# Kernel tuning notes

Hardware: AMD Instinct MI355X
Metric: run time of the kernel (lower is better)

Reference implementation:

```python
import jax, jax.numpy as jnp
import numpy as np

B, T = 16, 2048
OBS_DIM, ACT_DIM, HIDDEN = 64, 16, 512


def setup_inputs() -> dict:
    key = jax.random.key(0)
    ks = jax.random.split(key, 6)
    n = lambda k, shape, scale: (jax.random.normal(k, shape, dtype=jnp.float32) * scale)
    return {
        "obs": n(ks[0], (B, T, OBS_DIM), 1.0),
        "act": n(ks[1], (B, T, ACT_DIM), 1.0),
        "W_e": n(ks[2], (HIDDEN, OBS_DIM + ACT_DIM), 0.05),   # embed Linear weight
        "b_e": jnp.zeros((HIDDEN,), jnp.float32),             # embed Linear bias
        "a_raw": n(ks[3], (HIDDEN,), 0.5),                    # diagonal decay (pre-tanh)
        "W_B": n(ks[4], (HIDDEN, HIDDEN), 0.02),              # B Linear weight (no bias)
        "W_out": n(ks[5], (OBS_DIM, HIDDEN), 0.04),           # out Linear weight
        "b_out": jnp.zeros((OBS_DIM,), jnp.float32),          # out Linear bias
    }


def reference(obs, act, W_e, b_e, a_raw, W_B, W_out, b_out):
    # x: [B, T, obs+act]
    x = jnp.concatenate([obs, act], axis=-1)
    # embed: Linear + ReLU, batched over all timesteps -> u: [B, T, H]
    u = jax.nn.relu(jnp.einsum('btd,hd->bth', x, W_e) + b_e)
    # B projection batched over all t (the per-step matmul in the torch loop)
    v = jnp.einsum('bth,gh->btg', u, W_B)  # [B, T, H]
    a = jnp.tanh(a_raw)  # [H]
    # Diagonal linear recurrence s_t = a * s_{t-1} + v_t, s_0 starting from zeros,
    # realized as a parallel (log-depth) associative scan over (decay, input) pairs.
    A = jnp.broadcast_to(a, v.shape)
    def combine(c1, c2):
        a1, b1 = c1
        a2, b2 = c2
        return (a1 * a2, a2 * b1 + b2)
    _, s = jax.lax.associative_scan(combine, (A, v), axis=1)  # s: [B, T, H]
    # out projection per step -> preds: [B, T, obs_dim]
    return jnp.einsum('bth,oh->bto', s, W_out) + b_out
```

## Files before the change

kernel.cpp:

```cpp
#include <hip/hip_runtime.h>
#include <hip/hip_bf16.h>

#define B_    16
#define T_    2048
#define H_    512
#define BT_   32768
#define DIN   80
#define DPAD  128
#define L_    64
#define C_    32
#define O_    64
#define NCHUNK (BT_ / L_)

typedef __attribute__((ext_vector_type(8))) short short8;
typedef __attribute__((ext_vector_type(4))) float f32x4;
typedef __attribute__((ext_vector_type(4))) float float4v;

__device__ __forceinline__ float bf2f(unsigned short u) {
  union { unsigned int i; float f; } x; x.i = ((unsigned int)u) << 16; return x.f;
}
__device__ __forceinline__ unsigned short f2bf(float f) {
  union { float f; unsigned int i; } x; x.f = f;
  unsigned int r = x.i + 0x7fffu + ((x.i >> 16) & 1u);
  return (unsigned short)(r >> 16);
}

template<int NT, int RELU, int BIAS, int CE>
__global__ __launch_bounds__(512) void gemm256(
    const unsigned short* __restrict__ A, const unsigned short* __restrict__ Bt,
    const float* __restrict__ bias, unsigned short* __restrict__ Cb,
    int ldk,
    const float* __restrict__ powa,
    float* __restrict__ e)
{
  __shared__ __align__(16) unsigned char lds[131072];

  const int tid  = threadIdx.x;
  const int lane = tid & 63;
  const int wid  = tid >> 6;
  const int wr   = wid >> 2;
  const int wc   = wid & 3;
  const int cl   = lane & 15;
  const int kgrp = lane >> 4;
  const int rg   = kgrp * 4;

  const int X  = (int)blockIdx.x & 7;
  const int j  = (int)blockIdx.x >> 3;
  const int mt = X * 16 + (j >> 1);
  const int nt = j & 1;
  const int row0 = mt * 256, col0 = nt * 256;

  auto stageA = [&](int q, int buf) {
    const int k0 = q * 64;
    #pragma unroll
    for (int r = 0; r < 4; ++r) {
      const int o   = r * 8192 + tid * 16;
      const int row = o >> 7;
      const int c16 = (o >> 4) & 7;
      const int kk  = (c16 ^ (row & 7)) << 3;
      __builtin_amdgcn_global_load_lds(
          (const __attribute__((address_space(1))) void*)
              (A + (size_t)(row0 + row) * ldk + k0 + kk),
          (__attribute__((address_space(3))) void*)(lds + buf * 65536 + o),
          16, 0, 0);
    }
  };
  auto stageB = [&](int q, int buf) {
    const int k0 = q * 64;
    #pragma unroll
    for (int r = 0; r < 4; ++r) {
      const int o   = r * 8192 + tid * 16;
      const int col = o >> 7;
      const int c16 = (o >> 4) & 7;
      const int kk  = (c16 ^ (col & 7)) << 3;
      __builtin_amdgcn_global_load_lds(
          (const __attribute__((address_space(1))) void*)
              (Bt + (size_t)(col0 + col) * ldk + k0 + kk),
          (__attribute__((address_space(3))) void*)(lds + buf * 65536 + 32768 + o),
          16, 0, 0);
    }
  };

  f32x4 acc[8][4];
  #pragma unroll
  for (int m = 0; m < 8; ++m)
    #pragma unroll
    for (int n = 0; n < 4; ++n) acc[m][n] = f32x4{0.f, 0.f, 0.f, 0.f};

  stageA(0, 0); stageB(0, 0); stageB(1, 1);
  asm volatile("s_waitcnt vmcnt(4)" ::: "memory");
  __builtin_amdgcn_sched_barrier(0);
  __builtin_amdgcn_s_barrier();

  for (int q = 0; q < NT; ++q) {
    const int cur = q & 1;
    const unsigned char* bufp = lds + cur * 65536;

    if (q + 1 < NT) stageA(q + 1, cur ^ 1);

    short8 bfr[4][2];
    #pragma unroll
    for (int n = 0; n < 4; ++n) {
      const int col = wc * 64 + n * 16 + cl;
      #pragma unroll
      for (int ks = 0; ks < 2; ++ks)
        bfr[n][ks] = *(const short8*)(bufp + 32768 + col * 128 +
                                      ((((ks << 2) + kgrp) ^ (col & 7)) << 4));
    }
    asm volatile("s_waitcnt lgkmcnt(0)" ::: "memory");
    __builtin_amdgcn_sched_barrier(0);
    __builtin_amdgcn_s_barrier();

    if (q + 2 < NT) stageB(q + 2, cur);

    #pragma unroll
    for (int g = 0; g < 4; ++g) {
      short8 af[2][2];
      #pragma unroll
      for (int mm = 0; mm < 2; ++mm) {
        const int row = wr * 128 + (g * 2 + mm) * 16 + cl;
        #pragma unroll
        for (int ks = 0; ks < 2; ++ks)
          af[mm][ks] = *(const short8*)(bufp + row * 128 +
                                        ((((ks << 2) + kgrp) ^ (row & 7)) << 4));
      }
      #pragma unroll
      for (int ks = 0; ks < 2; ++ks)
        #pragma unroll
        for (int mm = 0; mm < 2; ++mm)
          #pragma unroll
          for (int n = 0; n < 4; ++n)
            acc[g * 2 + mm][n] = __builtin_amdgcn_mfma_f32_16x16x32_bf16(
                af[mm][ks], bfr[n][ks], acc[g * 2 + mm][n], 0, 0, 0);
    }

    if (q + 2 < NT) {
      asm volatile("s_waitcnt vmcnt(4)" ::: "memory");
    } else if (q + 1 < NT) {
      asm volatile("s_waitcnt vmcnt(0)" ::: "memory");
    }
    __builtin_amdgcn_sched_barrier(0);
    __builtin_amdgcn_s_barrier();
  }

  #pragma unroll
  for (int m = 0; m < 8; ++m) {
    #pragma unroll
    for (int n = 0; n < 4; ++n) {
      const int gc = col0 + wc * 64 + n * 16 + cl;
      #pragma unroll
      for (int e2 = 0; e2 < 4; ++e2) {
        const int gr = row0 + wr * 128 + m * 16 + rg + e2;
        float v = acc[m][n][e2];
        if (BIAS) v += bias[gc];
        if (RELU) v = fmaxf(v, 0.f);
        Cb[(size_t)gr * H_ + gc] = f2bf(v);
      }
    }
  }

  if (CE) {
    #pragma unroll
    for (int c = 0; c < 2; ++c) {
      const int chunk = ((row0 + wr * 128) >> 6) + c;
      #pragma unroll
      for (int n = 0; n < 4; ++n) {
        const int h = col0 + wc * 64 + n * 16 + cl;
        const float a16 = powa[15 * H_ + h];
        float ep = 0.f;
        #pragma unroll
        for (int e2 = 0; e2 < 4; ++e2) {
          const int k = 15 - rg - e2;
          const float wk = (k == 0) ? 1.f : powa[(size_t)(k - 1) * H_ + h];
          float hsum = acc[c * 4 + 0][n][e2];
          hsum = fmaf(hsum, a16, acc[c * 4 + 1][n][e2]);
          hsum = fmaf(hsum, a16, acc[c * 4 + 2][n][e2]);
          hsum = fmaf(hsum, a16, acc[c * 4 + 3][n][e2]);
          ep = fmaf(wk, hsum, ep);
        }
        ep += __shfl_xor(ep, 16);
        ep += __shfl_xor(ep, 32);
        if (kgrp == 0)
          e[(size_t)chunk * H_ + h] = ep;
      }
    }
  }
}

#define PX_N  (BT_ * 16)
#define WE_N  (H_ * DPAD)
#define WB_N  (H_ * H_)
#define WO_N  (O_ * H_)
#define PW_N  (WE_N + WB_N + WO_N + H_)
#define PREP_THREADS (PX_N + PW_N)

__global__ __launch_bounds__(256) void prep(
    const float* __restrict__ obs, const float* __restrict__ act,
    const float* __restrict__ W_e, const float* __restrict__ W_B,
    const float* __restrict__ W_out, const float* __restrict__ a_raw,
    unsigned short* __restrict__ xb,
    unsigned short* __restrict__ Web, unsigned short* __restrict__ WBb,
    unsigned short* __restrict__ Woutb, float* __restrict__ aarr,
    float* __restrict__ powa)
{
  const int gid = blockIdx.x * 256 + threadIdx.x;
  if (gid < PX_N) {
    const int g = gid & 15, n = gid >> 4;
    float f[8];
    if (g < 8) {
      const float4v f0 = ((const float4v*)obs)[(size_t)n * 16 + g * 2];
      const float4v f1 = ((const float4v*)obs)[(size_t)n * 16 + g * 2 + 1];
      f[0]=f0[0]; f[1]=f0[1]; f[2]=f0[2]; f[3]=f0[3];
      f[4]=f1[0]; f[5]=f1[1]; f[6]=f1[2]; f[7]=f1[3];
    } else if (g < 10) {
      const float4v f0 = ((const float4v*)act)[(size_t)n * 4 + (g - 8) * 2];
      const float4v f1 = ((const float4v*)act)[(size_t)n * 4 + (g - 8) * 2 + 1];
      f[0]=f0[0]; f[1]=f0[1]; f[2]=f0[2]; f[3]=f0[3];
      f[4]=f1[0]; f[5]=f1[1]; f[6]=f1[2]; f[7]=f1[3];
    } else {
      #pragma unroll
      for (int i = 0; i < 8; ++i) f[i] = 0.f;
    }
    short8 o;
    #pragma unroll
    for (int i = 0; i < 8; ++i) o[i] = (short)f2bf(f[i]);
    *(short8*)(xb + (size_t)gid * 8) = o;
    return;
  }
  const int idx = gid - PX_N;
  if (idx < WE_N) {
    const int h = idx >> 7, d = idx & 127;
    Web[idx] = f2bf(d < DIN ? W_e[h * DIN + d] : 0.f);
  } else if (idx < WE_N + WB_N) {
    const int j = idx - WE_N;
    WBb[j] = f2bf(W_B[j]);
  } else if (idx < WE_N + WB_N + WO_N) {
    const int j = idx - (WE_N + WB_N);
    Woutb[j] = f2bf(W_out[j]);
  } else if (idx < PW_N) {
    const int h = idx - (WE_N + WB_N + WO_N);
    const float a = tanhf(a_raw[h]);
    aarr[h] = a;
    float p = a;
    #pragma unroll
    for (int i = 0; i < 16; ++i) { powa[i * H_ + h] = p; p *= a; }
  }
}

__global__ __launch_bounds__(256) void scan_out(
    const unsigned int* __restrict__ v,
    const float* __restrict__ e,
    const float* __restrict__ aarr,
    const unsigned short* __restrict__ Wo,
    const float* __restrict__ b_out,
    float* __restrict__ y)
{
  __shared__ __align__(16) unsigned char sbytes[64 * 1024];
  const int blk = blockIdx.x;
  const int b = blk >> 5, c = blk & 31;
  const int tid = threadIdx.x;
  const int lane = tid & 63, w = tid >> 6;
  const int row_base = blk * L_;

  {
    const int h0 = tid * 2;
    const float a0 = aarr[h0], a1 = aarr[h0 + 1];
    float aL0 = a0 * a0, aL1 = a1 * a1;
    aL0 *= aL0; aL1 *= aL1;
    aL0 *= aL0; aL1 *= aL1;
    aL0 *= aL0; aL1 *= aL1;
    aL0 *= aL0; aL1 *= aL1;
    aL0 *= aL0; aL1 *= aL1;
    float s0 = 0.f, s1 = 0.f;
    for (int j = 0; j < c; ++j) {
      const size_t o = ((size_t)(b * C_ + j)) * H_ + h0;
      s0 = fmaf(aL0, s0, e[o]);
      s1 = fmaf(aL1, s1, e[o + 1]);
    }
    const unsigned int* vp = v + (size_t)row_base * (H_ / 2) + tid;
    #pragma unroll 8
    for (int t = 0; t < L_; ++t) {
      const unsigned int pv = vp[(size_t)t * (H_ / 2)];
      s0 = fmaf(a0, s0, bf2f((unsigned short)(pv & 0xffff)));
      s1 = fmaf(a1, s1, bf2f((unsigned short)(pv >> 16)));
      const int byte = t * 1024 + ((tid * 4) ^ ((t & 7) << 4));
      *(unsigned int*)(sbytes + byte) =
          (unsigned int)f2bf(s0) | ((unsigned int)f2bf(s1) << 16);
    }
  }
  __syncthreads();

  f32x4 acc[4];
  #pragma unroll
  for (int n = 0; n < 4; ++n) acc[n] = f32x4{0.f, 0.f, 0.f, 0.f};
  const int r = w * 16 + (lane & 15);
  const int kof = (lane >> 4) * 8;
  #pragma unroll 4
  for (int k0 = 0; k0 < H_; k0 += 32) {
    const int byte = r * 1024 + (((k0 + kof) * 2) ^ ((r & 7) << 4));
    const short8 af = *(const short8*)(sbytes + byte);
    #pragma unroll
    for (int n = 0; n < 4; ++n) {
      const short8 bf = *(const short8*)(Wo + (size_t)(n * 16 + (lane & 15)) * H_ + k0 + kof);
      acc[n] = __builtin_amdgcn_mfma_f32_16x16x32_bf16(af, bf, acc[n], 0, 0, 0);
    }
  }
  const int cl = lane & 15, rg = (lane >> 4) * 4;
  #pragma unroll
  for (int n = 0; n < 4; ++n) {
    #pragma unroll
    for (int e2 = 0; e2 < 4; ++e2) {
      const int gr = row_base + w * 16 + rg + e2;
      const int gc = n * 16 + cl;
      y[(size_t)gr * O_ + gc] = acc[n][e2] + b_out[gc];
    }
  }
}

extern "C" void kernel_launch(void* const* d_in, const int* in_sizes, int n_in,
                              void* d_out, int out_size, void* d_ws, size_t ws_size,
                              hipStream_t stream)
{
  const float* obs   = (const float*)d_in[0];
  const float* act   = (const float*)d_in[1];
  const float* W_e   = (const float*)d_in[2];
  const float* b_e   = (const float*)d_in[3];
  const float* a_raw = (const float*)d_in[4];
  const float* W_B   = (const float*)d_in[5];
  const float* W_out = (const float*)d_in[6];
  const float* b_out = (const float*)d_in[7];
  float* y = (float*)d_out;

  char* w = (char*)d_ws;
  auto carve = [&](size_t bytes) {
    char* p = w; w += (bytes + 255) & ~(size_t)255; return p;
  };
  unsigned short* xb    = (unsigned short*)carve((size_t)BT_ * DPAD * 2);
  unsigned short* Web   = (unsigned short*)carve((size_t)H_ * DPAD * 2);
  unsigned short* WBb   = (unsigned short*)carve((size_t)H_ * H_ * 2);
  unsigned short* Woutb = (unsigned short*)carve((size_t)O_ * H_ * 2);
  float*          aarr  = (float*)carve((size_t)H_ * 4);
  float*          powa  = (float*)carve((size_t)16 * H_ * 4);
  unsigned short* u     = (unsigned short*)carve((size_t)BT_ * H_ * 2);
  unsigned short* v     = (unsigned short*)carve((size_t)BT_ * H_ * 2);
  float*          e     = (float*)carve((size_t)NCHUNK * H_ * 4);

  prep<<<PREP_THREADS / 256, 256, 0, stream>>>(obs, act, W_e, W_B, W_out,
                                               a_raw, xb, Web, WBb, Woutb,
                                               aarr, powa);
  gemm256<2, 1, 1, 0><<<256, 512, 0, stream>>>(
      xb, Web, b_e, u, DPAD, nullptr, nullptr);
  gemm256<8, 0, 0, 1><<<256, 512, 0, stream>>>(
      u, WBb, nullptr, v, H_, powa, e);
  scan_out<<<NCHUNK, 256, 0, stream>>>((const unsigned int*)v, e, aarr,
                                       Woutb, b_out, y);
}
```

Baseline: 75.52 us.

## Fuse input conversion into embed GEMM, add carry-scan kernel, interleave B loads

The separate obs/act-to-bf16 prep pass and its xb buffer are removed. The embed GEMM now reads fp32 obs/act directly, converts them into swizzled LDS, and loads both K-tiles of W_e up front. The B-projection GEMM splits its B staging into per-round loads interleaved with the MFMA groups and raises wave priority around the compute. A new carry_scan kernel computes the per-chunk prefix states once, replacing the O(C) serial loop in every scan_out block, at the cost of an extra launch and buffer.

```diff
diff --git a/kernel.cpp b/kernel.cpp
--- a/kernel.cpp
+++ b/kernel.cpp
@@ -25,14 +25,13 @@
   return (unsigned short)(r >> 16);
 }
 
-template<int NT, int RELU, int BIAS, int CE>
-__global__ __launch_bounds__(512) void gemm256(
+__global__ __launch_bounds__(512) void gemm_bproj(
     const unsigned short* __restrict__ A, const unsigned short* __restrict__ Bt,
-    const float* __restrict__ bias, unsigned short* __restrict__ Cb,
-    int ldk,
+    unsigned short* __restrict__ Cb,
     const float* __restrict__ powa,
     float* __restrict__ e)
 {
+  constexpr int NT = 8;
   __shared__ __align__(16) unsigned char lds[131072];
 
   const int tid  = threadIdx.x;
@@ -60,13 +59,204 @@
       const int kk  = (c16 ^ (row & 7)) << 3;
       __builtin_amdgcn_global_load_lds(
           (const __attribute__((address_space(1))) void*)
-              (A + (size_t)(row0 + row) * ldk + k0 + kk),
+              (A + (size_t)(row0 + row) * H_ + k0 + kk),
           (__attribute__((address_space(3))) void*)(lds + buf * 65536 + o),
           16, 0, 0);
     }
   };
-  auto stageB = [&](int q, int buf) {
+  auto stageB_round = [&](int q, int buf, int r) {
     const int k0 = q * 64;
+    const int o   = r * 8192 + tid * 16;
+    const int col = o >> 7;
+    const int c16 = (o >> 4) & 7;
+    const int kk  = (c16 ^ (col & 7)) << 3;
+    __builtin_amdgcn_global_load_lds(
+        (const __attribute__((address_space(1))) void*)
+            (Bt + (size_t)(col0 + col) * H_ + k0 + kk),
+        (__attribute__((address_space(3))) void*)(lds + buf * 65536 + 32768 + o),
+        16, 0, 0);
+  };
+
+  f32x4 acc[8][4];
+  #pragma unroll
+  for (int m = 0; m < 8; ++m)
+    #pragma unroll
+    for (int n = 0; n < 4; ++n) acc[m][n] = f32x4{0.f, 0.f, 0.f, 0.f};
+
+  stageA(0, 0);
+  #pragma unroll
+  for (int r = 0; r < 4; ++r) stageB_round(0, 0, r);
+  #pragma unroll
+  for (int r = 0; r < 4; ++r) stageB_round(1, 1, r);
+  asm volatile("s_waitcnt vmcnt(4)" ::: "memory");
+  __builtin_amdgcn_sched_barrier(0);
+  __builtin_amdgcn_s_barrier();
+
+  for (int q = 0; q < NT; ++q) {
+    const int cur = q & 1;
+    const unsigned char* bufp = lds + cur * 65536;
+
+    if (q + 1 < NT) stageA(q + 1, cur ^ 1);
+
+    short8 bfr[4][2];
+    #pragma unroll
+    for (int n = 0; n < 4; ++n) {
+      const int col = wc * 64 + n * 16 + cl;
+      #pragma unroll
+      for (int ks = 0; ks < 2; ++ks)
+        bfr[n][ks] = *(const short8*)(bufp + 32768 + col * 128 +
+                                      ((((ks << 2) + kgrp) ^ (col & 7)) << 4));
+    }
+    asm volatile("s_waitcnt lgkmcnt(0)" ::: "memory");
+    __builtin_amdgcn_sched_barrier(0);
+    __builtin_amdgcn_s_barrier();
+
+    __builtin_amdgcn_s_setprio(1);
+    #pragma unroll
+    for (int g = 0; g < 4; ++g) {
+      if (q + 2 < NT) stageB_round(q + 2, cur, g);
+      short8 af[2][2];
+      #pragma unroll
+      for (int mm = 0; mm < 2; ++mm) {
+        const int row = wr * 128 + (g * 2 + mm) * 16 + cl;
+        #pragma unroll
+        for (int ks = 0; ks < 2; ++ks)
+          af[mm][ks] = *(const short8*)(bufp + row * 128 +
+                                        ((((ks << 2) + kgrp) ^ (row & 7)) << 4));
+      }
+      #pragma unroll
+      for (int ks = 0; ks < 2; ++ks)
+        #pragma unroll
+        for (int mm = 0; mm < 2; ++mm)
+          #pragma unroll
+          for (int n = 0; n < 4; ++n)
+            acc[g * 2 + mm][n] = __builtin_amdgcn_mfma_f32_16x16x32_bf16(
+                af[mm][ks], bfr[n][ks], acc[g * 2 + mm][n], 0, 0, 0);
+    }
+    __builtin_amdgcn_s_setprio(0);
+
+    if (q + 2 < NT) {
+      asm volatile("s_waitcnt vmcnt(4)" ::: "memory");
+    } else if (q + 1 < NT) {
+      asm volatile("s_waitcnt vmcnt(0)" ::: "memory");
+    }
+    __builtin_amdgcn_sched_barrier(0);
+    __builtin_amdgcn_s_barrier();
+  }
+
+  #pragma unroll
+  for (int m = 0; m < 8; ++m) {
+    #pragma unroll
+    for (int n = 0; n < 4; ++n) {
+      const int gc = col0 + wc * 64 + n * 16 + cl;
+      #pragma unroll
+      for (int e2 = 0; e2 < 4; ++e2) {
+        const int gr = row0 + wr * 128 + m * 16 + rg + e2;
+        Cb[(size_t)gr * H_ + gc] = f2bf(acc[m][n][e2]);
+      }
+    }
+  }
+
+  #pragma unroll
+  for (int c = 0; c < 2; ++c) {
+    const int chunk = ((row0 + wr * 128) >> 6) + c;
+    #pragma unroll
+    for (int n = 0; n < 4; ++n) {
+      const int h = col0 + wc * 64 + n * 16 + cl;
+      const float a16 = powa[15 * H_ + h];
+      float ep = 0.f;
+      #pragma unroll
+      for (int e2 = 0; e2 < 4; ++e2) {
+        const int k = 15 - rg - e2;
+        const float wk = (k == 0) ? 1.f : powa[(size_t)(k - 1) * H_ + h];
+        float hsum = acc[c * 4 + 0][n][e2];
+        hsum = fmaf(hsum, a16, acc[c * 4 + 1][n][e2]);
+        hsum = fmaf(hsum, a16, acc[c * 4 + 2][n][e2]);
+        hsum = fmaf(hsum, a16, acc[c * 4 + 3][n][e2]);
+        ep = fmaf(wk, hsum, ep);
+      }
+      ep += __shfl_xor(ep, 16);
+      ep += __shfl_xor(ep, 32);
+      if (kgrp == 0)
+        e[(size_t)chunk * H_ + h] = ep;
+    }
+  }
+}
+
+__global__ __launch_bounds__(512) void embed_gemm(
+    const float* __restrict__ obs, const float* __restrict__ act,
+    const unsigned short* __restrict__ Web,
+    const float* __restrict__ b_e,
+    unsigned short* __restrict__ u)
+{
+  __shared__ __align__(16) unsigned char lds[131072];
+
+  const int tid  = threadIdx.x;
+  const int lane = tid & 63;
+  const int wid  = tid >> 6;
+  const int wr   = wid >> 2;
+  const int wc   = wid & 3;
+  const int cl   = lane & 15;
+  const int kgrp = lane >> 4;
+  const int rg   = kgrp * 4;
+
+  const int X  = (int)blockIdx.x & 7;
+  const int j  = (int)blockIdx.x >> 3;
+  const int mt = X * 16 + (j >> 1);
+  const int nt = j & 1;
+  const int row0 = mt * 256, col0 = nt * 256;
+
+  {
+    const int row  = tid >> 1;
+    const int half = tid & 1;
+    {
+      const float4v* src = (const float4v*)(obs + (size_t)(row0 + row) * 64 + half * 32);
+      float f[32];
+      #pragma unroll
+      for (int i = 0; i < 8; ++i) {
+        const float4v t4 = src[i];
+        f[i*4+0]=t4[0]; f[i*4+1]=t4[1]; f[i*4+2]=t4[2]; f[i*4+3]=t4[3];
+      }
+      #pragma unroll
+      for (int cc = 0; cc < 4; ++cc) {
+        short8 o8;
+        #pragma unroll
+        for (int jj = 0; jj < 8; ++jj) o8[jj] = (short)f2bf(f[cc*8+jj]);
+        const int c16 = half * 4 + cc;
+        *(short8*)(lds + row * 128 + ((c16 ^ (row & 7)) << 4)) = o8;
+      }
+    }
+    {
+      short8 z8;
+      #pragma unroll
+      for (int jj = 0; jj < 8; ++jj) z8[jj] = 0;
+      if (half == 0) {
+        const float4v* asrc = (const float4v*)(act + (size_t)(row0 + row) * 16);
+        float g[16];
+        #pragma unroll
+        for (int i = 0; i < 4; ++i) {
+          const float4v t4 = asrc[i];
+          g[i*4+0]=t4[0]; g[i*4+1]=t4[1]; g[i*4+2]=t4[2]; g[i*4+3]=t4[3];
+        }
+        #pragma unroll
+        for (int cc = 0; cc < 2; ++cc) {
+          short8 o8;
+          #pragma unroll
+          for (int jj = 0; jj < 8; ++jj) o8[jj] = (short)f2bf(g[cc*8+jj]);
+          *(short8*)(lds + 65536 + row * 128 + ((cc ^ (row & 7)) << 4)) = o8;
+        }
+        #pragma unroll
+        for (int cc = 2; cc < 4; ++cc)
+          *(short8*)(lds + 65536 + row * 128 + ((cc ^ (row & 7)) << 4)) = z8;
+      } else {
+        #pragma unroll
+        for (int cc = 4; cc < 8; ++cc)
+          *(short8*)(lds + 65536 + row * 128 + ((cc ^ (row & 7)) << 4)) = z8;
+      }
+    }
+  }
+  #pragma unroll
+  for (int q = 0; q < 2; ++q) {
     #pragma unroll
     for (int r = 0; r < 4; ++r) {
       const int o   = r * 8192 + tid * 16;
@@ -75,11 +265,12 @@
       const int kk  = (c16 ^ (col & 7)) << 3;
       __builtin_amdgcn_global_load_lds(
           (const __attribute__((address_space(1))) void*)
-              (Bt + (size_t)(col0 + col) * ldk + k0 + kk),
-          (__attribute__((address_space(3))) void*)(lds + buf * 65536 + 32768 + o),
+              (Web + (size_t)(col0 + col) * DPAD + q * 64 + kk),
+          (__attribute__((address_space(3))) void*)(lds + q * 65536 + 32768 + o),
           16, 0, 0);
     }
-  };
+  }
+  __syncthreads();
 
   f32x4 acc[8][4];
   #pragma unroll
@@ -87,17 +278,9 @@
     #pragma unroll
     for (int n = 0; n < 4; ++n) acc[m][n] = f32x4{0.f, 0.f, 0.f, 0.f};
 
-  stageA(0, 0); stageB(0, 0); stageB(1, 1);
-  asm volatile("s_waitcnt vmcnt(4)" ::: "memory");
-  __builtin_amdgcn_sched_barrier(0);
-  __builtin_amdgcn_s_barrier();
-
-  for (int q = 0; q < NT; ++q) {
-    const int cur = q & 1;
-    const unsigned char* bufp = lds + cur * 65536;
-
-    if (q + 1 < NT) stageA(q + 1, cur ^ 1);
-
+  #pragma unroll
+  for (int q = 0; q < 2; ++q) {
+    const unsigned char* bufp = lds + q * 65536;
     short8 bfr[4][2];
     #pragma unroll
     for (int n = 0; n < 4; ++n) {
@@ -107,12 +290,6 @@
         bfr[n][ks] = *(const short8*)(bufp + 32768 + col * 128 +
                                       ((((ks << 2) + kgrp) ^ (col & 7)) << 4));
     }
-    asm volatile("s_waitcnt lgkmcnt(0)" ::: "memory");
-    __builtin_amdgcn_sched_barrier(0);
-    __builtin_amdgcn_s_barrier();
-
-    if (q + 2 < NT) stageB(q + 2, cur);
-
     #pragma unroll
     for (int g = 0; g < 4; ++g) {
       short8 af[2][2];
@@ -133,14 +310,6 @@
             acc[g * 2 + mm][n] = __builtin_amdgcn_mfma_f32_16x16x32_bf16(
                 af[mm][ks], bfr[n][ks], acc[g * 2 + mm][n], 0, 0, 0);
     }
-
-    if (q + 2 < NT) {
-      asm volatile("s_waitcnt vmcnt(4)" ::: "memory");
-    } else if (q + 1 < NT) {
-      asm volatile("s_waitcnt vmcnt(0)" ::: "memory");
-    }
-    __builtin_amdgcn_sched_barrier(0);
-    __builtin_amdgcn_s_barrier();
   }
 
   #pragma unroll
@@ -148,95 +317,38 @@
     #pragma unroll
     for (int n = 0; n < 4; ++n) {
       const int gc = col0 + wc * 64 + n * 16 + cl;
+      const float be = b_e[gc];
       #pragma unroll
       for (int e2 = 0; e2 < 4; ++e2) {
         const int gr = row0 + wr * 128 + m * 16 + rg + e2;
-        float v = acc[m][n][e2];
-        if (BIAS) v += bias[gc];
-        if (RELU) v = fmaxf(v, 0.f);
-        Cb[(size_t)gr * H_ + gc] = f2bf(v);
-      }
-    }
-  }
-
-  if (CE) {
-    #pragma unroll
-    for (int c = 0; c < 2; ++c) {
-      const int chunk = ((row0 + wr * 128) >> 6) + c;
-      #pragma unroll
-      for (int n = 0; n < 4; ++n) {
-        const int h = col0 + wc * 64 + n * 16 + cl;
-        const float a16 = powa[15 * H_ + h];
-        float ep = 0.f;
-        #pragma unroll
-        for (int e2 = 0; e2 < 4; ++e2) {
-          const int k = 15 - rg - e2;
-          const float wk = (k == 0) ? 1.f : powa[(size_t)(k - 1) * H_ + h];
-          float hsum = acc[c * 4 + 0][n][e2];
-          hsum = fmaf(hsum, a16, acc[c * 4 + 1][n][e2]);
-          hsum = fmaf(hsum, a16, acc[c * 4 + 2][n][e2]);
-          hsum = fmaf(hsum, a16, acc[c * 4 + 3][n][e2]);
-          ep = fmaf(wk, hsum, ep);
-        }
-        ep += __shfl_xor(ep, 16);
-        ep += __shfl_xor(ep, 32);
-        if (kgrp == 0)
-          e[(size_t)chunk * H_ + h] = ep;
-      }
-    }
-  }
-}
-
-#define PX_N  (BT_ * 16)
+        u[(size_t)gr * H_ + gc] = f2bf(fmaxf(acc[m][n][e2] + be, 0.f));
+      }
+    }
+  }
+}
+
 #define WE_N  (H_ * DPAD)
 #define WB_N  (H_ * H_)
 #define WO_N  (O_ * H_)
 #define PW_N  (WE_N + WB_N + WO_N + H_)
-#define PREP_THREADS (PX_N + PW_N)
-
-__global__ __launch_bounds__(256) void prep(
-    const float* __restrict__ obs, const float* __restrict__ act,
+
+__global__ __launch_bounds__(256) void prep_w(
     const float* __restrict__ W_e, const float* __restrict__ W_B,
     const float* __restrict__ W_out, const float* __restrict__ a_raw,
-    unsigned short* __restrict__ xb,
     unsigned short* __restrict__ Web, unsigned short* __restrict__ WBb,
     unsigned short* __restrict__ Woutb, float* __restrict__ aarr,
     float* __restrict__ powa)
 {
-  const int gid = blockIdx.x * 256 + threadIdx.x;
-  if (gid < PX_N) {
-    const int g = gid & 15, n = gid >> 4;
-    float f[8];
-    if (g < 8) {
-      const float4v f0 = ((const float4v*)obs)[(size_t)n * 16 + g * 2];
-      const float4v f1 = ((const float4v*)obs)[(size_t)n * 16 + g * 2 + 1];
-      f[0]=f0[0]; f[1]=f0[1]; f[2]=f0[2]; f[3]=f0[3];
-      f[4]=f1[0]; f[5]=f1[1]; f[6]=f1[2]; f[7]=f1[3];
-    } else if (g < 10) {
-      const float4v f0 = ((const float4v*)act)[(size_t)n * 4 + (g - 8) * 2];
-      const float4v f1 = ((const float4v*)act)[(size_t)n * 4 + (g - 8) * 2 + 1];
-      f[0]=f0[0]; f[1]=f0[1]; f[2]=f0[2]; f[3]=f0[3];
-      f[4]=f1[0]; f[5]=f1[1]; f[6]=f1[2]; f[7]=f1[3];
-    } else {
-      #pragma unroll
-      for (int i = 0; i < 8; ++i) f[i] = 0.f;
-    }
-    short8 o;
-    #pragma unroll
-    for (int i = 0; i < 8; ++i) o[i] = (short)f2bf(f[i]);
-    *(short8*)(xb + (size_t)gid * 8) = o;
-    return;
-  }
-  const int idx = gid - PX_N;
+  const int idx = blockIdx.x * 256 + threadIdx.x;
   if (idx < WE_N) {
     const int h = idx >> 7, d = idx & 127;
     Web[idx] = f2bf(d < DIN ? W_e[h * DIN + d] : 0.f);
   } else if (idx < WE_N + WB_N) {
-    const int j = idx - WE_N;
-    WBb[j] = f2bf(W_B[j]);
+    const int j2 = idx - WE_N;
+    WBb[j2] = f2bf(W_B[j2]);
   } else if (idx < WE_N + WB_N + WO_N) {
-    const int j = idx - (WE_N + WB_N);
-    Woutb[j] = f2bf(W_out[j]);
+    const int j2 = idx - (WE_N + WB_N);
+    Woutb[j2] = f2bf(W_out[j2]);
   } else if (idx < PW_N) {
     const int h = idx - (WE_N + WB_N + WO_N);
     const float a = tanhf(a_raw[h]);
@@ -247,9 +359,29 @@
   }
 }
 
+__global__ __launch_bounds__(256) void carry_scan(
+    const float* __restrict__ e, float* __restrict__ P,
+    const float* __restrict__ aarr)
+{
+  const int idx = blockIdx.x * 256 + threadIdx.x;
+  const int b = idx >> 9, h = idx & (H_ - 1);
+  const float a = aarr[h];
+  float aL = a * a; aL *= aL; aL *= aL; aL *= aL; aL *= aL; aL *= aL;
+  float ev[C_];
+  #pragma unroll
+  for (int c = 0; c < C_; ++c)
+    ev[c] = e[((size_t)(b * C_ + c)) * H_ + h];
+  float S = 0.f;
+  #pragma unroll
+  for (int c = 0; c < C_; ++c) {
+    P[((size_t)(b * C_ + c)) * H_ + h] = S;
+    S = fmaf(aL, S, ev[c]);
+  }
+}
+
 __global__ __launch_bounds__(256) void scan_out(
     const unsigned int* __restrict__ v,
-    const float* __restrict__ e,
+    const float* __restrict__ P,
     const float* __restrict__ aarr,
     const unsigned short* __restrict__ Wo,
     const float* __restrict__ b_out,
@@ -257,7 +389,6 @@
 {
   __shared__ __align__(16) unsigned char sbytes[64 * 1024];
   const int blk = blockIdx.x;
-  const int b = blk >> 5, c = blk & 31;
   const int tid = threadIdx.x;
   const int lane = tid & 63, w = tid >> 6;
   const int row_base = blk * L_;
@@ -265,18 +396,8 @@
   {
     const int h0 = tid * 2;
     const float a0 = aarr[h0], a1 = aarr[h0 + 1];
-    float aL0 = a0 * a0, aL1 = a1 * a1;
-    aL0 *= aL0; aL1 *= aL1;
-    aL0 *= aL0; aL1 *= aL1;
-    aL0 *= aL0; aL1 *= aL1;
-    aL0 *= aL0; aL1 *= aL1;
-    aL0 *= aL0; aL1 *= aL1;
-    float s0 = 0.f, s1 = 0.f;
-    for (int j = 0; j < c; ++j) {
-      const size_t o = ((size_t)(b * C_ + j)) * H_ + h0;
-      s0 = fmaf(aL0, s0, e[o]);
-      s1 = fmaf(aL1, s1, e[o + 1]);
-    }
+    float s0 = P[(size_t)blk * H_ + h0];
+    float s1 = P[(size_t)blk * H_ + h0 + 1];
     const unsigned int* vp = v + (size_t)row_base * (H_ / 2) + tid;
     #pragma unroll 8
     for (int t = 0; t < L_; ++t) {
@@ -335,7 +456,6 @@
   auto carve = [&](size_t bytes) {
     char* p = w; w += (bytes + 255) & ~(size_t)255; return p;
   };
-  unsigned short* xb    = (unsigned short*)carve((size_t)BT_ * DPAD * 2);
   unsigned short* Web   = (unsigned short*)carve((size_t)H_ * DPAD * 2);
   unsigned short* WBb   = (unsigned short*)carve((size_t)H_ * H_ * 2);
   unsigned short* Woutb = (unsigned short*)carve((size_t)O_ * H_ * 2);
@@ -344,14 +464,13 @@
   unsigned short* u     = (unsigned short*)carve((size_t)BT_ * H_ * 2);
   unsigned short* v     = (unsigned short*)carve((size_t)BT_ * H_ * 2);
   float*          e     = (float*)carve((size_t)NCHUNK * H_ * 4);
-
-  prep<<<PREP_THREADS / 256, 256, 0, stream>>>(obs, act, W_e, W_B, W_out,
-                                               a_raw, xb, Web, WBb, Woutb,
-                                               aarr, powa);
-  gemm256<2, 1, 1, 0><<<256, 512, 0, stream>>>(
-      xb, Web, b_e, u, DPAD, nullptr, nullptr);
-  gemm256<8, 0, 0, 1><<<256, 512, 0, stream>>>(
-      u, WBb, nullptr, v, H_, powa, e);
-  scan_out<<<NCHUNK, 256, 0, stream>>>((const unsigned int*)v, e, aarr,
+  float*          P     = (float*)carve((size_t)NCHUNK * H_ * 4);
+
+  prep_w<<<PW_N / 256, 256, 0, stream>>>(W_e, W_B, W_out, a_raw,
+                                         Web, WBb, Woutb, aarr, powa);
+  embed_gemm<<<256, 512, 0, stream>>>(obs, act, Web, b_e, u);
+  gemm_bproj<<<256, 512, 0, stream>>>(u, WBb, v, powa, e);
+  carry_scan<<<(B_ * H_) / 256, 256, 0, stream>>>(e, P, aarr);
+  scan_out<<<NCHUNK, 256, 0, stream>>>((const unsigned int*)v, P, aarr,
                                        Woutb, b_out, y);
 }
```

Result: faster. 70.64 us (-6.5%).
